# Kernel tuning notes

Measured on AMD Instinct MI355X. Metric: run time of the kernel, lower is better.

The kernel has to match this reference:

```python
import jax, jax.numpy as jnp
import numpy as np

# model dims
C_CH = 64      # channels C
M_DIM = 128    # state dim m
R = 8          # low-rank r
DG = 64        # token_dim d_g
CHUNK = 512    # chunk_len
B, H, W = 4, 256, 256


def setup_inputs() -> dict:
    key = jax.random.key(0)
    ks = jax.random.split(key, 12)
    n = jax.random.normal
    return {
        "x": n(ks[0], (B, C_CH, H, W), jnp.float32),
        "g": n(ks[1], (B, DG), jnp.float32),
        # 1x1 conv weights flattened to matrices
        "in_proj_w": n(ks[2], (M_DIM, C_CH), jnp.float32) * 0.05,
        "in_proj_b": jnp.zeros((M_DIM,), jnp.float32),
        "out_proj_w": n(ks[3], (C_CH, M_DIM), jnp.float32) * 0.05,  # Cbase; conv bias unused in forward
        "U_base": n(ks[4], (M_DIM, R), jnp.float32) * 0.02,
        "V_base": n(ks[5], (M_DIM, R), jnp.float32) * 0.02,
        "a_base": jnp.zeros((M_DIM,), jnp.float32),
        "mod_uv_w": n(ks[6], (2 * R, DG), jnp.float32) * 0.05,
        "mod_uv_b": jnp.zeros((2 * R,), jnp.float32),
        "mod_a_w": n(ks[7], (M_DIM, DG), jnp.float32) * 0.05,
        "mod_a_b": jnp.zeros((M_DIM,), jnp.float32),
        "mod_B_w": n(ks[8], (M_DIM, DG), jnp.float32) * 0.05,
        "mod_B_b": jnp.zeros((M_DIM,), jnp.float32),
        "mod_C_w": n(ks[9], (C_CH, DG), jnp.float32) * 0.05,
        "mod_C_b": jnp.zeros((C_CH,), jnp.float32),
        "h0": jnp.zeros((M_DIM,), jnp.float32),
    }


def reference(x, g, in_proj_w, in_proj_b, out_proj_w, U_base, V_base, a_base,
              mod_uv_w, mod_uv_b, mod_a_w, mod_a_b, mod_B_w, mod_B_b,
              mod_C_w, mod_C_b, h0):
    Bsz, Cch, Hh, Ww = x.shape
    # 1x1 conv in_proj
    x_proj = jnp.einsum('bchw,mc->bmhw', x, in_proj_w) + in_proj_b[None, :, None, None]
    # g-conditioned modulations
    uv = g @ mod_uv_w.T + mod_uv_b
    gU = jnp.clip(uv[:, :R], -0.5, 0.5)[:, None, :]          # (B,1,r)
    gV = jnp.clip(uv[:, R:], -0.5, 0.5)[:, None, :]          # (B,1,r)
    ga = jnp.clip(g @ mod_a_w.T + mod_a_b, -2.0, 2.0)        # (B,m)
    gB = jnp.clip(g @ mod_B_w.T + mod_B_b, -1.0, 1.0)        # (B,m)
    gC = jnp.clip(g @ mod_C_w.T + mod_C_b, -0.5, 0.5)        # (B,C)
    Ug = U_base[None] * (1.0 + gU)                            # (B,m,r)
    Vg = V_base[None] * (1.0 + gV)                            # (B,m,r)
    a = a_base[None] + ga                                     # (B,m)
    Cg = out_proj_w[None] * (1.0 + gC)[:, :, None]            # (B,C,m)

    L = Hh * Ww
    x_seq = x_proj.reshape(Bsz, M_DIM, L).transpose(0, 2, 1)  # (B,L,m)
    x_seq = x_seq * (1.0 + gB)[:, None, :]
    pad = (-L) % CHUNK
    if pad > 0:
        x_seq = jnp.pad(x_seq, ((0, 0), (0, pad), (0, 0)))
    Lp = L + pad
    Mch = Lp // CHUNK
    # (T, B, K, m): scan over time within chunks, chunks run in parallel
    x_chunks = x_seq.reshape(Bsz, Mch, CHUNK, M_DIM).transpose(2, 0, 1, 3)
    h_init = jnp.broadcast_to(h0, (Bsz, Mch, M_DIM))

    def step(h, xt):
        v = jnp.einsum('bmr,bkm->bkr', Vg, h)                 # V^T h
        Av = jnp.einsum('bmr,bkr->bkm', Ug, v)                # U (V^T h)
        h_new = jnp.clip(Av + h * a[:, None, :] + xt, -10.0, 10.0)
        yc = jnp.clip(jnp.einsum('bcm,bkm->bkc', Cg, h_new), -10.0, 10.0)
        return h_new, yc

    _, ys = jax.lax.scan(step, h_init, x_chunks)              # (T,B,K,C)
    out_flat = ys.transpose(1, 2, 0, 3).reshape(Bsz, Lp, Cch)[:, :L, :]
    return out_flat.transpose(0, 2, 1).reshape(Bsz, Cch, Hh, Ww)
```

## Files before the change

kernel.cpp:

```cpp
#include <hip/hip_runtime.h>
#include <hip/hip_fp16.h>

#define L_TOT 65536

#define WS_UG   0
#define WS_VG   4096
#define WS_A    8192
#define WS_GB1  8704
#define WS_WHP  12288
#define WS_WLP  16384
#define WS_CGP  32768
#define WS_XS   65536

typedef __attribute__((ext_vector_type(8))) short short8;
typedef __attribute__((ext_vector_type(4))) float f32x4;

__device__ __forceinline__ unsigned bf16rne(float f) {
    unsigned u = __builtin_bit_cast(unsigned, f);
    return (u + 0x7fffu + ((u >> 16) & 1u)) >> 16;
}
__device__ __forceinline__ float bfhi(unsigned u) {
    return __builtin_bit_cast(float, u << 16);
}

#define DPP_ROW(CT) \
    "v_add_f32_dpp %0, %0, %0 " CT "\n\t" \
    "v_add_f32_dpp %1, %1, %1 " CT "\n\t" \
    "v_add_f32_dpp %2, %2, %2 " CT "\n\t" \
    "v_add_f32_dpp %3, %3, %3 " CT "\n\t" \
    "v_add_f32_dpp %4, %4, %4 " CT "\n\t" \
    "v_add_f32_dpp %5, %5, %5 " CT "\n\t" \
    "v_add_f32_dpp %6, %6, %6 " CT "\n\t" \
    "v_add_f32_dpp %7, %7, %7 " CT "\n\t"

__global__ __launch_bounds__(128) void mod_kernel(
    const float* __restrict__ g, const float* __restrict__ in_proj_w,
    const float* __restrict__ U_base, const float* __restrict__ V_base,
    const float* __restrict__ a_base, const float* __restrict__ out_proj_w,
    const float* __restrict__ mod_uv_w, const float* __restrict__ mod_uv_b,
    const float* __restrict__ mod_a_w, const float* __restrict__ mod_a_b,
    const float* __restrict__ mod_B_w, const float* __restrict__ mod_B_b,
    const float* __restrict__ mod_C_w, const float* __restrict__ mod_C_b,
    float* __restrict__ ws)
{
    __shared__ float gsh[64];
    __shared__ float uvs[16];
    __shared__ float gCs[64];
    const int b = blockIdx.x, tid = threadIdx.x;
    if (tid < 64) gsh[tid] = g[b * 64 + tid];
    __syncthreads();
    if (tid < 16) {
        float s = mod_uv_b[tid];
        for (int d = 0; d < 64; ++d) s += mod_uv_w[tid * 64 + d] * gsh[d];
        uvs[tid] = fminf(0.5f, fmaxf(-0.5f, s));
    }
    float ga_v, gB_v;
    {
        float s = mod_a_b[tid];
        for (int d = 0; d < 64; ++d) s += mod_a_w[tid * 64 + d] * gsh[d];
        ga_v = fminf(2.0f, fmaxf(-2.0f, s));
    }
    {
        float s = mod_B_b[tid];
        for (int d = 0; d < 64; ++d) s += mod_B_w[tid * 64 + d] * gsh[d];
        gB_v = 1.0f + fminf(1.0f, fmaxf(-1.0f, s));
    }
    if (tid < 64) {
        float s = mod_C_b[tid];
        for (int d = 0; d < 64; ++d) s += mod_C_w[tid * 64 + d] * gsh[d];
        gCs[tid] = 1.0f + fminf(0.5f, fmaxf(-0.5f, s));
    }
    __syncthreads();
    for (int idx = tid; idx < 1024; idx += 128) {
        int m = idx >> 3, r = idx & 7;
        ws[WS_UG + (b * 128 + m) * 8 + r] = U_base[m * 8 + r] * (1.0f + uvs[r]);
        ws[WS_VG + (b * 128 + m) * 8 + r] = V_base[m * 8 + r] * (1.0f + uvs[8 + r]);
    }
    ws[WS_A   + b * 128 + tid] = a_base[tid] + ga_v;
    ws[WS_GB1 + b * 128 + tid] = gB_v;
    unsigned* CgP = (unsigned*)(ws + WS_CGP);
    for (int idx = tid; idx < 4096; idx += 128) {
        int c = idx >> 6, j = idx & 63;
        float s = gCs[c];
        float c0 = out_proj_w[c * 128 + 2 * j]     * s;
        float c1 = out_proj_w[c * 128 + 2 * j + 1] * s;
        CgP[(b * 64 + c) * 64 + j] = bf16rne(c0) | (bf16rne(c1) << 16);
    }
    if (b == 0) {
        unsigned* WhP = (unsigned*)(ws + WS_WHP);
        unsigned* WlP = (unsigned*)(ws + WS_WLP);
        for (int idx = tid; idx < 4096; idx += 128) {
            int m = idx >> 5, j = idx & 31;
            float w0 = in_proj_w[m * 64 + 2 * j];
            float w1 = in_proj_w[m * 64 + 2 * j + 1];
            unsigned u0 = bf16rne(w0), u1 = bf16rne(w1);
            WhP[idx] = u0 | (u1 << 16);
            float r0 = w0 - bfhi(u0);
            float r1 = w1 - bfhi(u1);
            WlP[idx] = bf16rne(r0) | (bf16rne(r1) << 16);
        }
    }
}

__global__ __launch_bounds__(256) void inproj_mfma(
    const float* __restrict__ x, const unsigned* __restrict__ WhP,
    const unsigned* __restrict__ WlP, const float* __restrict__ bias,
    const float* __restrict__ ws, unsigned* __restrict__ xs16)
{
    __shared__ __align__(16) unsigned XhS[64 * 36];
    __shared__ __align__(16) unsigned XlS[64 * 36];
    const int tid = threadIdx.x;
    const int b = blockIdx.y;
    const int l0 = blockIdx.x * 64;

    {
        const int l_st = tid & 63, cpg = tid >> 6;
        #pragma unroll
        for (int s = 0; s < 8; ++s) {
            int cp = cpg * 8 + s;
            float x0 = x[(size_t)(b * 64 + 2 * cp) * L_TOT + l0 + l_st];
            float x1 = x[(size_t)(b * 64 + 2 * cp + 1) * L_TOT + l0 + l_st];
            unsigned u0 = bf16rne(x0), u1 = bf16rne(x1);
            XhS[l_st * 36 + cp] = u0 | (u1 << 16);
            float r0 = x0 - bfhi(u0);
            float r1 = x1 - bfhi(u1);
            XlS[l_st * 36 + cp] = bf16rne(r0) | (bf16rne(r1) << 16);
        }
    }
    const int lane = tid & 63, wv = tid >> 6;
    const int row16 = lane & 15, grp = lane >> 4;

    short8 Ah[2][2], Al[2][2];
    #pragma unroll
    for (int t = 0; t < 2; ++t) {
        const int mrow = (2 * wv + t) * 16 + row16;
        #pragma unroll
        for (int kc = 0; kc < 2; ++kc) {
            Ah[t][kc] = __builtin_bit_cast(short8,
                *(const uint4*)(WhP + mrow * 32 + kc * 16 + grp * 4));
            Al[t][kc] = __builtin_bit_cast(short8,
                *(const uint4*)(WlP + mrow * 32 + kc * 16 + grp * 4));
        }
    }
    __syncthreads();

    #pragma unroll
    for (int ti = 0; ti < 4; ++ti) {
        const int lcol = ti * 16 + row16;
        short8 Bh[2], Bl[2];
        #pragma unroll
        for (int kc = 0; kc < 2; ++kc) {
            Bh[kc] = __builtin_bit_cast(short8,
                *(const uint4*)&XhS[lcol * 36 + kc * 16 + grp * 4]);
            Bl[kc] = __builtin_bit_cast(short8,
                *(const uint4*)&XlS[lcol * 36 + kc * 16 + grp * 4]);
        }
        #pragma unroll
        for (int t = 0; t < 2; ++t) {
            f32x4 acc = {0.f, 0.f, 0.f, 0.f};
            acc = __builtin_amdgcn_mfma_f32_16x16x32_bf16(Ah[t][0], Bh[0], acc, 0, 0, 0);
            acc = __builtin_amdgcn_mfma_f32_16x16x32_bf16(Ah[t][1], Bh[1], acc, 0, 0, 0);
            acc = __builtin_amdgcn_mfma_f32_16x16x32_bf16(Ah[t][0], Bl[0], acc, 0, 0, 0);
            acc = __builtin_amdgcn_mfma_f32_16x16x32_bf16(Ah[t][1], Bl[1], acc, 0, 0, 0);
            acc = __builtin_amdgcn_mfma_f32_16x16x32_bf16(Al[t][0], Bh[0], acc, 0, 0, 0);
            acc = __builtin_amdgcn_mfma_f32_16x16x32_bf16(Al[t][1], Bh[1], acc, 0, 0, 0);
            const int mb = (2 * wv + t) * 16 + 4 * grp;
            const int l = l0 + lcol;
            float4 bi = *(const float4*)(bias + mb);
            float4 gb = *(const float4*)(ws + WS_GB1 + b * 128 + mb);
            float v0 = (acc[0] + bi.x) * gb.x;
            float v1 = (acc[1] + bi.y) * gb.y;
            float v2 = (acc[2] + bi.z) * gb.z;
            float v3 = (acc[3] + bi.w) * gb.w;
            __half2 h01 = __floats2half2_rn(v0, v1);
            __half2 h23 = __floats2half2_rn(v2, v3);
            uint2 pk = {__builtin_bit_cast(unsigned, h01), __builtin_bit_cast(unsigned, h23)};
            *(uint2*)(xs16 + ((size_t)b * L_TOT + l) * 64 + (mb >> 1)) = pk;
        }
    }
}

__global__ __launch_bounds__(64, 1) void scan_kernel(
    const unsigned* __restrict__ xs16, const float* __restrict__ ws,
    const unsigned* __restrict__ CgP, const float* __restrict__ h0,
    float* __restrict__ out)
{
    __shared__ __align__(16) unsigned Hs[16 * 68];
    const int lane = threadIdx.x;
    const int bb = blockIdx.x >> 7, k = blockIdx.x & 127;
    const int m0 = 2 * lane;

    float Vg0[8], Vg1[8], Ug0[8], Ug1[8];
    {
        const float* vg = ws + WS_VG + (bb * 128 + m0) * 8;
        const float* ug = ws + WS_UG + (bb * 128 + m0) * 8;
        #pragma unroll
        for (int r = 0; r < 8; ++r) {
            Vg0[r] = vg[r]; Vg1[r] = vg[8 + r];
            Ug0[r] = ug[r]; Ug1[r] = ug[8 + r];
        }
    }
    const float a0 = ws[WS_A + bb * 128 + m0];
    const float a1 = ws[WS_A + bb * 128 + m0 + 1];
    float ha = h0[m0], hb = h0[m0 + 1];

    short8 Af[4][4];
    const int row16 = lane & 15, grp = lane >> 4;
    #pragma unroll
    for (int ct = 0; ct < 4; ++ct)
        #pragma unroll
        for (int kc = 0; kc < 4; ++kc) {
            const unsigned* p = CgP + (bb * 64 + ct * 16 + row16) * 64 + kc * 16 + grp * 4;
            Af[ct][kc] = __builtin_bit_cast(short8, *(const uint4*)p);
        }

    const unsigned* xsp = xs16 + ((size_t)bb * L_TOT + (size_t)k * 512) * 64 + lane;
    float* ob[4];
    #pragma unroll
    for (int ct = 0; ct < 4; ++ct)
        ob[ct] = out + (size_t)(bb * 64 + ct * 16 + grp * 4) * L_TOT + k * 512 + row16;

    unsigned xqA[16], xqB[16];

    auto prefetch = [&](unsigned (&xq)[16], int seg) {
        const unsigned* xb = xsp + (size_t)seg * 1024;
        #pragma unroll
        for (int i = 0; i < 16; ++i) xq[i] = xb[(size_t)i * 64];
    };
    auto do_seg = [&](const unsigned (&xq)[16], int t16) {
        #pragma unroll
        for (int i = 0; i < 16; ++i) {
            const float2 xv = __half22float2(__builtin_bit_cast(__half2, xq[i]));
            float p0 = fmaf(Vg1[0], hb, Vg0[0] * ha);
            float p1 = fmaf(Vg1[1], hb, Vg0[1] * ha);
            float p2 = fmaf(Vg1[2], hb, Vg0[2] * ha);
            float p3 = fmaf(Vg1[3], hb, Vg0[3] * ha);
            float p4 = fmaf(Vg1[4], hb, Vg0[4] * ha);
            float p5 = fmaf(Vg1[5], hb, Vg0[5] * ha);
            float p6 = fmaf(Vg1[6], hb, Vg0[6] * ha);
            float p7 = fmaf(Vg1[7], hb, Vg0[7] * ha);
            asm volatile(
                "s_nop 1\n\t"
                DPP_ROW("quad_perm:[1,0,3,2] row_mask:0xf bank_mask:0xf bound_ctrl:1")
                DPP_ROW("quad_perm:[2,3,0,1] row_mask:0xf bank_mask:0xf bound_ctrl:1")
                DPP_ROW("row_half_mirror row_mask:0xf bank_mask:0xf bound_ctrl:1")
                DPP_ROW("row_mirror row_mask:0xf bank_mask:0xf bound_ctrl:1")
                DPP_ROW("row_bcast:15 row_mask:0xa bank_mask:0xf")
                DPP_ROW("row_bcast:31 row_mask:0xc bank_mask:0xf")
                : "+v"(p0), "+v"(p1), "+v"(p2), "+v"(p3),
                  "+v"(p4), "+v"(p5), "+v"(p6), "+v"(p7));
            float v0 = __builtin_bit_cast(float, __builtin_amdgcn_readlane(__builtin_bit_cast(int, p0), 63));
            float v1 = __builtin_bit_cast(float, __builtin_amdgcn_readlane(__builtin_bit_cast(int, p1), 63));
            float v2 = __builtin_bit_cast(float, __builtin_amdgcn_readlane(__builtin_bit_cast(int, p2), 63));
            float v3 = __builtin_bit_cast(float, __builtin_amdgcn_readlane(__builtin_bit_cast(int, p3), 63));
            float v4 = __builtin_bit_cast(float, __builtin_amdgcn_readlane(__builtin_bit_cast(int, p4), 63));
            float v5 = __builtin_bit_cast(float, __builtin_amdgcn_readlane(__builtin_bit_cast(int, p5), 63));
            float v6 = __builtin_bit_cast(float, __builtin_amdgcn_readlane(__builtin_bit_cast(int, p6), 63));
            float v7 = __builtin_bit_cast(float, __builtin_amdgcn_readlane(__builtin_bit_cast(int, p7), 63));
            float q0 = fmaf(v1, Ug0[1], v0 * Ug0[0]);
            float q1 = fmaf(v3, Ug0[3], v2 * Ug0[2]);
            float q2 = fmaf(v5, Ug0[5], v4 * Ug0[4]);
            float q3 = fmaf(v7, Ug0[7], v6 * Ug0[6]);
            float av0 = (q0 + q1) + (q2 + q3);
            float s0 = fmaf(v1, Ug1[1], v0 * Ug1[0]);
            float s1 = fmaf(v3, Ug1[3], v2 * Ug1[2]);
            float s2 = fmaf(v5, Ug1[5], v4 * Ug1[4]);
            float s3 = fmaf(v7, Ug1[7], v6 * Ug1[6]);
            float av1 = (s0 + s1) + (s2 + s3);
            ha = fminf(10.0f, fmaxf(-10.0f, fmaf(a0, ha, av0) + xv.x));
            hb = fminf(10.0f, fmaxf(-10.0f, fmaf(a1, hb, av1) + xv.y));
            unsigned hp;
            asm("v_cvt_pk_bf16_f32 %0, %1, %2" : "=v"(hp) : "v"(ha), "v"(hb));
            Hs[i * 68 + lane] = hp;
        }
        short8 Bf[4];
        #pragma unroll
        for (int kc = 0; kc < 4; ++kc)
            Bf[kc] = __builtin_bit_cast(short8,
                *(const uint4*)&Hs[row16 * 68 + kc * 16 + grp * 4]);
        #pragma unroll
        for (int ct = 0; ct < 4; ++ct) {
            f32x4 acc = {0.0f, 0.0f, 0.0f, 0.0f};
            #pragma unroll
            for (int kc = 0; kc < 4; ++kc)
                acc = __builtin_amdgcn_mfma_f32_16x16x32_bf16(Af[ct][kc], Bf[kc], acc, 0, 0, 0);
            #pragma unroll
            for (int r = 0; r < 4; ++r) {
                float y = fminf(10.0f, fmaxf(-10.0f, acc[r]));
                ob[ct][(size_t)r * L_TOT + t16 * 16] = y;
            }
        }
    };

    prefetch(xqA, 0);
    #pragma unroll 1
    for (int t16 = 0; t16 < 32; t16 += 2) {
        prefetch(xqB, t16 + 1);
        do_seg(xqA, t16);
        prefetch(xqA, (t16 + 2) & 31);
        do_seg(xqB, t16 + 1);
    }
}

extern "C" void kernel_launch(void* const* d_in, const int* in_sizes, int n_in,
                              void* d_out, int out_size, void* d_ws, size_t ws_size,
                              hipStream_t stream) {
    const float* x          = (const float*)d_in[0];
    const float* g          = (const float*)d_in[1];
    const float* in_proj_w  = (const float*)d_in[2];
    const float* in_proj_b  = (const float*)d_in[3];
    const float* out_proj_w = (const float*)d_in[4];
    const float* U_base     = (const float*)d_in[5];
    const float* V_base     = (const float*)d_in[6];
    const float* a_base     = (const float*)d_in[7];
    const float* mod_uv_w   = (const float*)d_in[8];
    const float* mod_uv_b   = (const float*)d_in[9];
    const float* mod_a_w    = (const float*)d_in[10];
    const float* mod_a_b    = (const float*)d_in[11];
    const float* mod_B_w    = (const float*)d_in[12];
    const float* mod_B_b    = (const float*)d_in[13];
    const float* mod_C_w    = (const float*)d_in[14];
    const float* mod_C_b    = (const float*)d_in[15];
    const float* h0         = (const float*)d_in[16];
    float* out = (float*)d_out;
    float* ws  = (float*)d_ws;
    unsigned* xs16 = (unsigned*)(ws + WS_XS);

    hipLaunchKernelGGL(mod_kernel, dim3(4), dim3(128), 0, stream,
                       g, in_proj_w, U_base, V_base, a_base, out_proj_w,
                       mod_uv_w, mod_uv_b, mod_a_w, mod_a_b,
                       mod_B_w, mod_B_b, mod_C_w, mod_C_b, ws);
    hipLaunchKernelGGL(inproj_mfma, dim3(1024, 4), dim3(256), 0, stream,
                       x, (const unsigned*)(ws + WS_WHP), (const unsigned*)(ws + WS_WLP),
                       in_proj_b, ws, xs16);
    hipLaunchKernelGGL(scan_kernel, dim3(512), dim3(64), 0, stream,
                       xs16, ws, (const unsigned*)(ws + WS_CGP), h0, out);
}
```

Before: 172.1 us.

## Fuse in-projection into scan kernel with warp-specialized producer/scan/output pipeline

Result: slower. 193.5 us (+12.4%).

```diff
diff --git a/kernel.cpp b/kernel.cpp
--- a/kernel.cpp
+++ b/kernel.cpp
@@ -10,7 +10,6 @@
 #define WS_WHP  12288
 #define WS_WLP  16384
 #define WS_CGP  32768
-#define WS_XS   65536
 
 typedef __attribute__((ext_vector_type(8))) short short8;
 typedef __attribute__((ext_vector_type(4))) float f32x4;
@@ -102,96 +101,26 @@
     }
 }
 
-__global__ __launch_bounds__(256) void inproj_mfma(
+__global__ __launch_bounds__(192, 1) void fused_kernel(
     const float* __restrict__ x, const unsigned* __restrict__ WhP,
     const unsigned* __restrict__ WlP, const float* __restrict__ bias,
-    const float* __restrict__ ws, unsigned* __restrict__ xs16)
+    const float* __restrict__ ws, const unsigned* __restrict__ CgP,
+    const float* __restrict__ h0, float* __restrict__ out)
 {
-    __shared__ __align__(16) unsigned XhS[64 * 36];
-    __shared__ __align__(16) unsigned XlS[64 * 36];
+    __shared__ __align__(16) unsigned XhS[16 * 36];
+    __shared__ __align__(16) unsigned XlS[16 * 36];
+    __shared__ __align__(16) unsigned xp[2][64 * 17];
+    __shared__ __align__(16) unsigned Hs[2][16 * 68];
+
     const int tid = threadIdx.x;
-    const int b = blockIdx.y;
-    const int l0 = blockIdx.x * 64;
-
-    {
-        const int l_st = tid & 63, cpg = tid >> 6;
-        #pragma unroll
-        for (int s = 0; s < 8; ++s) {
-            int cp = cpg * 8 + s;
-            float x0 = x[(size_t)(b * 64 + 2 * cp) * L_TOT + l0 + l_st];
-            float x1 = x[(size_t)(b * 64 + 2 * cp + 1) * L_TOT + l0 + l_st];
-            unsigned u0 = bf16rne(x0), u1 = bf16rne(x1);
-            XhS[l_st * 36 + cp] = u0 | (u1 << 16);
-            float r0 = x0 - bfhi(u0);
-            float r1 = x1 - bfhi(u1);
-            XlS[l_st * 36 + cp] = bf16rne(r0) | (bf16rne(r1) << 16);
-        }
-    }
-    const int lane = tid & 63, wv = tid >> 6;
+    const int lane = tid & 63, wid = tid >> 6;
+    const int bb = blockIdx.x >> 7, kchunk = blockIdx.x & 127;
+    const size_t l0chunk = (size_t)kchunk * 512;
     const int row16 = lane & 15, grp = lane >> 4;
 
-    short8 Ah[2][2], Al[2][2];
-    #pragma unroll
-    for (int t = 0; t < 2; ++t) {
-        const int mrow = (2 * wv + t) * 16 + row16;
-        #pragma unroll
-        for (int kc = 0; kc < 2; ++kc) {
-            Ah[t][kc] = __builtin_bit_cast(short8,
-                *(const uint4*)(WhP + mrow * 32 + kc * 16 + grp * 4));
-            Al[t][kc] = __builtin_bit_cast(short8,
-                *(const uint4*)(WlP + mrow * 32 + kc * 16 + grp * 4));
-        }
-    }
-    __syncthreads();
-
-    #pragma unroll
-    for (int ti = 0; ti < 4; ++ti) {
-        const int lcol = ti * 16 + row16;
-        short8 Bh[2], Bl[2];
-        #pragma unroll
-        for (int kc = 0; kc < 2; ++kc) {
-            Bh[kc] = __builtin_bit_cast(short8,
-                *(const uint4*)&XhS[lcol * 36 + kc * 16 + grp * 4]);
-            Bl[kc] = __builtin_bit_cast(short8,
-                *(const uint4*)&XlS[lcol * 36 + kc * 16 + grp * 4]);
-        }
-        #pragma unroll
-        for (int t = 0; t < 2; ++t) {
-            f32x4 acc = {0.f, 0.f, 0.f, 0.f};
-            acc = __builtin_amdgcn_mfma_f32_16x16x32_bf16(Ah[t][0], Bh[0], acc, 0, 0, 0);
-            acc = __builtin_amdgcn_mfma_f32_16x16x32_bf16(Ah[t][1], Bh[1], acc, 0, 0, 0);
-            acc = __builtin_amdgcn_mfma_f32_16x16x32_bf16(Ah[t][0], Bl[0], acc, 0, 0, 0);
-            acc = __builtin_amdgcn_mfma_f32_16x16x32_bf16(Ah[t][1], Bl[1], acc, 0, 0, 0);
-            acc = __builtin_amdgcn_mfma_f32_16x16x32_bf16(Al[t][0], Bh[0], acc, 0, 0, 0);
-            acc = __builtin_amdgcn_mfma_f32_16x16x32_bf16(Al[t][1], Bh[1], acc, 0, 0, 0);
-            const int mb = (2 * wv + t) * 16 + 4 * grp;
-            const int l = l0 + lcol;
-            float4 bi = *(const float4*)(bias + mb);
-            float4 gb = *(const float4*)(ws + WS_GB1 + b * 128 + mb);
-            float v0 = (acc[0] + bi.x) * gb.x;
-            float v1 = (acc[1] + bi.y) * gb.y;
-            float v2 = (acc[2] + bi.z) * gb.z;
-            float v3 = (acc[3] + bi.w) * gb.w;
-            __half2 h01 = __floats2half2_rn(v0, v1);
-            __half2 h23 = __floats2half2_rn(v2, v3);
-            uint2 pk = {__builtin_bit_cast(unsigned, h01), __builtin_bit_cast(unsigned, h23)};
-            *(uint2*)(xs16 + ((size_t)b * L_TOT + l) * 64 + (mb >> 1)) = pk;
-        }
-    }
-}
-
-__global__ __launch_bounds__(64, 1) void scan_kernel(
-    const unsigned* __restrict__ xs16, const float* __restrict__ ws,
-    const unsigned* __restrict__ CgP, const float* __restrict__ h0,
-    float* __restrict__ out)
-{
-    __shared__ __align__(16) unsigned Hs[16 * 68];
-    const int lane = threadIdx.x;
-    const int bb = blockIdx.x >> 7, k = blockIdx.x & 127;
+    float Vg0[8], Vg1[8], Ug0[8], Ug1[8], a0 = 0.f, a1 = 0.f, ha = 0.f, hb = 0.f;
     const int m0 = 2 * lane;
-
-    float Vg0[8], Vg1[8], Ug0[8], Ug1[8];
-    {
+    if (wid == 0) {
         const float* vg = ws + WS_VG + (bb * 128 + m0) * 8;
         const float* ug = ws + WS_UG + (bb * 128 + m0) * 8;
         #pragma unroll
@@ -199,106 +128,151 @@
             Vg0[r] = vg[r]; Vg1[r] = vg[8 + r];
             Ug0[r] = ug[r]; Ug1[r] = ug[8 + r];
         }
-    }
-    const float a0 = ws[WS_A + bb * 128 + m0];
-    const float a1 = ws[WS_A + bb * 128 + m0 + 1];
-    float ha = h0[m0], hb = h0[m0 + 1];
-
+        a0 = ws[WS_A + bb * 128 + m0];
+        a1 = ws[WS_A + bb * 128 + m0 + 1];
+        ha = h0[m0]; hb = h0[m0 + 1];
+    }
     short8 Af[4][4];
-    const int row16 = lane & 15, grp = lane >> 4;
-    #pragma unroll
-    for (int ct = 0; ct < 4; ++ct)
-        #pragma unroll
-        for (int kc = 0; kc < 4; ++kc) {
-            const unsigned* p = CgP + (bb * 64 + ct * 16 + row16) * 64 + kc * 16 + grp * 4;
-            Af[ct][kc] = __builtin_bit_cast(short8, *(const uint4*)p);
-        }
-
-    const unsigned* xsp = xs16 + ((size_t)bb * L_TOT + (size_t)k * 512) * 64 + lane;
     float* ob[4];
-    #pragma unroll
-    for (int ct = 0; ct < 4; ++ct)
-        ob[ct] = out + (size_t)(bb * 64 + ct * 16 + grp * 4) * L_TOT + k * 512 + row16;
-
-    unsigned xqA[16], xqB[16];
-
-    auto prefetch = [&](unsigned (&xq)[16], int seg) {
-        const unsigned* xb = xsp + (size_t)seg * 1024;
-        #pragma unroll
-        for (int i = 0; i < 16; ++i) xq[i] = xb[(size_t)i * 64];
-    };
-    auto do_seg = [&](const unsigned (&xq)[16], int t16) {
-        #pragma unroll
-        for (int i = 0; i < 16; ++i) {
-            const float2 xv = __half22float2(__builtin_bit_cast(__half2, xq[i]));
-            float p0 = fmaf(Vg1[0], hb, Vg0[0] * ha);
-            float p1 = fmaf(Vg1[1], hb, Vg0[1] * ha);
-            float p2 = fmaf(Vg1[2], hb, Vg0[2] * ha);
-            float p3 = fmaf(Vg1[3], hb, Vg0[3] * ha);
-            float p4 = fmaf(Vg1[4], hb, Vg0[4] * ha);
-            float p5 = fmaf(Vg1[5], hb, Vg0[5] * ha);
-            float p6 = fmaf(Vg1[6], hb, Vg0[6] * ha);
-            float p7 = fmaf(Vg1[7], hb, Vg0[7] * ha);
-            asm volatile(
-                "s_nop 1\n\t"
-                DPP_ROW("quad_perm:[1,0,3,2] row_mask:0xf bank_mask:0xf bound_ctrl:1")
-                DPP_ROW("quad_perm:[2,3,0,1] row_mask:0xf bank_mask:0xf bound_ctrl:1")
-                DPP_ROW("row_half_mirror row_mask:0xf bank_mask:0xf bound_ctrl:1")
-                DPP_ROW("row_mirror row_mask:0xf bank_mask:0xf bound_ctrl:1")
-                DPP_ROW("row_bcast:15 row_mask:0xa bank_mask:0xf")
-                DPP_ROW("row_bcast:31 row_mask:0xc bank_mask:0xf")
-                : "+v"(p0), "+v"(p1), "+v"(p2), "+v"(p3),
-                  "+v"(p4), "+v"(p5), "+v"(p6), "+v"(p7));
-            float v0 = __builtin_bit_cast(float, __builtin_amdgcn_readlane(__builtin_bit_cast(int, p0), 63));
-            float v1 = __builtin_bit_cast(float, __builtin_amdgcn_readlane(__builtin_bit_cast(int, p1), 63));
-            float v2 = __builtin_bit_cast(float, __builtin_amdgcn_readlane(__builtin_bit_cast(int, p2), 63));
-            float v3 = __builtin_bit_cast(float, __builtin_amdgcn_readlane(__builtin_bit_cast(int, p3), 63));
-            float v4 = __builtin_bit_cast(float, __builtin_amdgcn_readlane(__builtin_bit_cast(int, p4), 63));
-            float v5 = __builtin_bit_cast(float, __builtin_amdgcn_readlane(__builtin_bit_cast(int, p5), 63));
-            float v6 = __builtin_bit_cast(float, __builtin_amdgcn_readlane(__builtin_bit_cast(int, p6), 63));
-            float v7 = __builtin_bit_cast(float, __builtin_amdgcn_readlane(__builtin_bit_cast(int, p7), 63));
-            float q0 = fmaf(v1, Ug0[1], v0 * Ug0[0]);
-            float q1 = fmaf(v3, Ug0[3], v2 * Ug0[2]);
-            float q2 = fmaf(v5, Ug0[5], v4 * Ug0[4]);
-            float q3 = fmaf(v7, Ug0[7], v6 * Ug0[6]);
-            float av0 = (q0 + q1) + (q2 + q3);
-            float s0 = fmaf(v1, Ug1[1], v0 * Ug1[0]);
-            float s1 = fmaf(v3, Ug1[3], v2 * Ug1[2]);
-            float s2 = fmaf(v5, Ug1[5], v4 * Ug1[4]);
-            float s3 = fmaf(v7, Ug1[7], v6 * Ug1[6]);
-            float av1 = (s0 + s1) + (s2 + s3);
-            ha = fminf(10.0f, fmaxf(-10.0f, fmaf(a0, ha, av0) + xv.x));
-            hb = fminf(10.0f, fmaxf(-10.0f, fmaf(a1, hb, av1) + xv.y));
-            unsigned hp;
-            asm("v_cvt_pk_bf16_f32 %0, %1, %2" : "=v"(hp) : "v"(ha), "v"(hb));
-            Hs[i * 68 + lane] = hp;
-        }
-        short8 Bf[4];
-        #pragma unroll
-        for (int kc = 0; kc < 4; ++kc)
-            Bf[kc] = __builtin_bit_cast(short8,
-                *(const uint4*)&Hs[row16 * 68 + kc * 16 + grp * 4]);
+    if (wid == 2) {
         #pragma unroll
         for (int ct = 0; ct < 4; ++ct) {
-            f32x4 acc = {0.0f, 0.0f, 0.0f, 0.0f};
+            #pragma unroll
+            for (int kc = 0; kc < 4; ++kc) {
+                const unsigned* p = CgP + (bb * 64 + ct * 16 + row16) * 64 + kc * 16 + grp * 4;
+                Af[ct][kc] = __builtin_bit_cast(short8, *(const uint4*)p);
+            }
+            ob[ct] = out + (size_t)(bb * 64 + ct * 16 + grp * 4) * L_TOT + l0chunk + row16;
+        }
+    }
+
+    for (int k = -1; k <= 32; ++k) {
+        if (wid == 1 && k <= 30) {
+            const int s = k + 1;
+            const float* xb = x + (size_t)(bb * 64) * L_TOT + l0chunk + s * 16 + row16;
+            #pragma unroll
+            for (int t = 0; t < 8; ++t) {
+                int cp = grp * 8 + t;
+                float x0 = xb[(size_t)(2 * cp) * L_TOT];
+                float x1 = xb[(size_t)(2 * cp + 1) * L_TOT];
+                unsigned u0 = bf16rne(x0), u1 = bf16rne(x1);
+                XhS[row16 * 36 + cp] = u0 | (u1 << 16);
+                float r0 = x0 - bfhi(u0);
+                float r1 = x1 - bfhi(u1);
+                XlS[row16 * 36 + cp] = bf16rne(r0) | (bf16rne(r1) << 16);
+            }
+            asm volatile("s_waitcnt lgkmcnt(0)" ::: "memory");
+            short8 Bh[2], Bl[2];
+            #pragma unroll
+            for (int kc = 0; kc < 2; ++kc) {
+                Bh[kc] = __builtin_bit_cast(short8,
+                    *(const uint4*)&XhS[row16 * 36 + kc * 16 + grp * 4]);
+                Bl[kc] = __builtin_bit_cast(short8,
+                    *(const uint4*)&XlS[row16 * 36 + kc * 16 + grp * 4]);
+            }
+            unsigned* xpd = xp[s & 1];
+            #pragma unroll
+            for (int mt = 0; mt < 8; ++mt) {
+                const int mrow = mt * 16 + row16;
+                short8 Ah0 = __builtin_bit_cast(short8, *(const uint4*)(WhP + mrow * 32 + grp * 4));
+                short8 Ah1 = __builtin_bit_cast(short8, *(const uint4*)(WhP + mrow * 32 + 16 + grp * 4));
+                short8 Al0 = __builtin_bit_cast(short8, *(const uint4*)(WlP + mrow * 32 + grp * 4));
+                short8 Al1 = __builtin_bit_cast(short8, *(const uint4*)(WlP + mrow * 32 + 16 + grp * 4));
+                f32x4 acc = {0.f, 0.f, 0.f, 0.f};
+                acc = __builtin_amdgcn_mfma_f32_16x16x32_bf16(Ah0, Bh[0], acc, 0, 0, 0);
+                acc = __builtin_amdgcn_mfma_f32_16x16x32_bf16(Ah1, Bh[1], acc, 0, 0, 0);
+                acc = __builtin_amdgcn_mfma_f32_16x16x32_bf16(Ah0, Bl[0], acc, 0, 0, 0);
+                acc = __builtin_amdgcn_mfma_f32_16x16x32_bf16(Ah1, Bl[1], acc, 0, 0, 0);
+                acc = __builtin_amdgcn_mfma_f32_16x16x32_bf16(Al0, Bh[0], acc, 0, 0, 0);
+                acc = __builtin_amdgcn_mfma_f32_16x16x32_bf16(Al1, Bh[1], acc, 0, 0, 0);
+                const int mb = mt * 16 + 4 * grp;
+                float4 bi = *(const float4*)(bias + mb);
+                float4 gb = *(const float4*)(ws + WS_GB1 + bb * 128 + mb);
+                float v0 = (acc[0] + bi.x) * gb.x;
+                float v1 = (acc[1] + bi.y) * gb.y;
+                float v2 = (acc[2] + bi.z) * gb.z;
+                float v3 = (acc[3] + bi.w) * gb.w;
+                __half2 h01 = __floats2half2_rn(v0, v1);
+                __half2 h23 = __floats2half2_rn(v2, v3);
+                const int mp = mb >> 1;
+                xpd[mp * 17 + row16]       = __builtin_bit_cast(unsigned, h01);
+                xpd[(mp + 1) * 17 + row16] = __builtin_bit_cast(unsigned, h23);
+            }
+        }
+        if (wid == 0 && k >= 0 && k <= 31) {
+            const unsigned* xpk = xp[k & 1];
+            unsigned* Hk = Hs[k & 1];
+            unsigned xq[16];
+            #pragma unroll
+            for (int i = 0; i < 16; ++i) xq[i] = xpk[lane * 17 + i];
+            #pragma unroll
+            for (int i = 0; i < 16; ++i) {
+                const float2 xv = __half22float2(__builtin_bit_cast(__half2, xq[i]));
+                float p0 = fmaf(Vg1[0], hb, Vg0[0] * ha);
+                float p1 = fmaf(Vg1[1], hb, Vg0[1] * ha);
+                float p2 = fmaf(Vg1[2], hb, Vg0[2] * ha);
+                float p3 = fmaf(Vg1[3], hb, Vg0[3] * ha);
+                float p4 = fmaf(Vg1[4], hb, Vg0[4] * ha);
+                float p5 = fmaf(Vg1[5], hb, Vg0[5] * ha);
+                float p6 = fmaf(Vg1[6], hb, Vg0[6] * ha);
+                float p7 = fmaf(Vg1[7], hb, Vg0[7] * ha);
+                asm volatile(
+                    "s_nop 1\n\t"
+                    DPP_ROW("quad_perm:[1,0,3,2] row_mask:0xf bank_mask:0xf bound_ctrl:1")
+                    DPP_ROW("quad_perm:[2,3,0,1] row_mask:0xf bank_mask:0xf bound_ctrl:1")
+                    DPP_ROW("row_half_mirror row_mask:0xf bank_mask:0xf bound_ctrl:1")
+                    DPP_ROW("row_mirror row_mask:0xf bank_mask:0xf bound_ctrl:1")
+                    DPP_ROW("row_bcast:15 row_mask:0xa bank_mask:0xf")
+                    DPP_ROW("row_bcast:31 row_mask:0xc bank_mask:0xf")
+                    : "+v"(p0), "+v"(p1), "+v"(p2), "+v"(p3),
+                      "+v"(p4), "+v"(p5), "+v"(p6), "+v"(p7));
+                float v0 = __builtin_bit_cast(float, __builtin_amdgcn_readlane(__builtin_bit_cast(int, p0), 63));
+                float v1 = __builtin_bit_cast(float, __builtin_amdgcn_readlane(__builtin_bit_cast(int, p1), 63));
+                float v2 = __builtin_bit_cast(float, __builtin_amdgcn_readlane(__builtin_bit_cast(int, p2), 63));
+                float v3 = __builtin_bit_cast(float, __builtin_amdgcn_readlane(__builtin_bit_cast(int, p3), 63));
+                float v4 = __builtin_bit_cast(float, __builtin_amdgcn_readlane(__builtin_bit_cast(int, p4), 63));
+                float v5 = __builtin_bit_cast(float, __builtin_amdgcn_readlane(__builtin_bit_cast(int, p5), 63));
+                float v6 = __builtin_bit_cast(float, __builtin_amdgcn_readlane(__builtin_bit_cast(int, p6), 63));
+                float v7 = __builtin_bit_cast(float, __builtin_amdgcn_readlane(__builtin_bit_cast(int, p7), 63));
+                float q0 = fmaf(v1, Ug0[1], v0 * Ug0[0]);
+                float q1 = fmaf(v3, Ug0[3], v2 * Ug0[2]);
+                float q2 = fmaf(v5, Ug0[5], v4 * Ug0[4]);
+                float q3 = fmaf(v7, Ug0[7], v6 * Ug0[6]);
+                float av0 = (q0 + q1) + (q2 + q3);
+                float s0 = fmaf(v1, Ug1[1], v0 * Ug1[0]);
+                float s1 = fmaf(v3, Ug1[3], v2 * Ug1[2]);
+                float s2 = fmaf(v5, Ug1[5], v4 * Ug1[4]);
+                float s3 = fmaf(v7, Ug1[7], v6 * Ug1[6]);
+                float av1 = (s0 + s1) + (s2 + s3);
+                ha = fminf(10.0f, fmaxf(-10.0f, fmaf(a0, ha, av0) + xv.x));
+                hb = fminf(10.0f, fmaxf(-10.0f, fmaf(a1, hb, av1) + xv.y));
+                unsigned hp;
+                asm("v_cvt_pk_bf16_f32 %0, %1, %2" : "=v"(hp) : "v"(ha), "v"(hb));
+                Hk[i * 68 + lane] = hp;
+            }
+        }
+        if (wid == 2 && k >= 1) {
+            const int s = k - 1;
+            const unsigned* Hp = Hs[s & 1];
+            short8 Bf[4];
             #pragma unroll
             for (int kc = 0; kc < 4; ++kc)
-                acc = __builtin_amdgcn_mfma_f32_16x16x32_bf16(Af[ct][kc], Bf[kc], acc, 0, 0, 0);
-            #pragma unroll
-            for (int r = 0; r < 4; ++r) {
-                float y = fminf(10.0f, fmaxf(-10.0f, acc[r]));
-                ob[ct][(size_t)r * L_TOT + t16 * 16] = y;
-            }
-        }
-    };
-
-    prefetch(xqA, 0);
-    #pragma unroll 1
-    for (int t16 = 0; t16 < 32; t16 += 2) {
-        prefetch(xqB, t16 + 1);
-        do_seg(xqA, t16);
-        prefetch(xqA, (t16 + 2) & 31);
-        do_seg(xqB, t16 + 1);
+                Bf[kc] = __builtin_bit_cast(short8,
+                    *(const uint4*)&Hp[row16 * 68 + kc * 16 + grp * 4]);
+            #pragma unroll
+            for (int ct = 0; ct < 4; ++ct) {
+                f32x4 acc = {0.0f, 0.0f, 0.0f, 0.0f};
+                #pragma unroll
+                for (int kc = 0; kc < 4; ++kc)
+                    acc = __builtin_amdgcn_mfma_f32_16x16x32_bf16(Af[ct][kc], Bf[kc], acc, 0, 0, 0);
+                #pragma unroll
+                for (int r = 0; r < 4; ++r) {
+                    float y = fminf(10.0f, fmaxf(-10.0f, acc[r]));
+                    ob[ct][(size_t)r * L_TOT + s * 16] = y;
+                }
+            }
+        }
+        __syncthreads();
     }
 }
 
@@ -324,15 +298,12 @@
     const float* h0         = (const float*)d_in[16];
     float* out = (float*)d_out;
     float* ws  = (float*)d_ws;
-    unsigned* xs16 = (unsigned*)(ws + WS_XS);
 
     hipLaunchKernelGGL(mod_kernel, dim3(4), dim3(128), 0, stream,
                        g, in_proj_w, U_base, V_base, a_base, out_proj_w,
                        mod_uv_w, mod_uv_b, mod_a_w, mod_a_b,
                        mod_B_w, mod_B_b, mod_C_w, mod_C_b, ws);
-    hipLaunchKernelGGL(inproj_mfma, dim3(1024, 4), dim3(256), 0, stream,
+    hipLaunchKernelGGL(fused_kernel, dim3(512), dim3(192), 0, stream,
                        x, (const unsigned*)(ws + WS_WHP), (const unsigned*)(ws + WS_WLP),
-                       in_proj_b, ws, xs16);
-    hipLaunchKernelGGL(scan_kernel, dim3(512), dim3(64), 0, stream,
-                       xs16, ws, (const unsigned*)(ws + WS_CGP), h0, out);
-}
+                       in_proj_b, ws, (const unsigned*)(ws + WS_CGP), h0, out);
+}
```

## Compute per-step V^T h with split-fp16 MFMA instead of DPP reductions

Applied to the files above, without the earlier changes.

Result: slower. 188.3 us (+9.4%).

```diff
diff --git a/kernel.cpp b/kernel.cpp
--- a/kernel.cpp
+++ b/kernel.cpp
@@ -14,6 +14,7 @@
 
 typedef __attribute__((ext_vector_type(8))) short short8;
 typedef __attribute__((ext_vector_type(4))) float f32x4;
+typedef _Float16 half8 __attribute__((ext_vector_type(8)));
 
 __device__ __forceinline__ unsigned bf16rne(float f) {
     unsigned u = __builtin_bit_cast(unsigned, f);
@@ -22,16 +23,10 @@
 __device__ __forceinline__ float bfhi(unsigned u) {
     return __builtin_bit_cast(float, u << 16);
 }
-
-#define DPP_ROW(CT) \
-    "v_add_f32_dpp %0, %0, %0 " CT "\n\t" \
-    "v_add_f32_dpp %1, %1, %1 " CT "\n\t" \
-    "v_add_f32_dpp %2, %2, %2 " CT "\n\t" \
-    "v_add_f32_dpp %3, %3, %3 " CT "\n\t" \
-    "v_add_f32_dpp %4, %4, %4 " CT "\n\t" \
-    "v_add_f32_dpp %5, %5, %5 " CT "\n\t" \
-    "v_add_f32_dpp %6, %6, %6 " CT "\n\t" \
-    "v_add_f32_dpp %7, %7, %7 " CT "\n\t"
+__device__ __forceinline__ unsigned f16pk(float a, float b) {
+    __half2 h = __floats2half2_rn(a, b);
+    return __builtin_bit_cast(unsigned, h);
+}
 
 __global__ __launch_bounds__(128) void mod_kernel(
     const float* __restrict__ g, const float* __restrict__ in_proj_w,
@@ -84,7 +79,7 @@
         float s = gCs[c];
         float c0 = out_proj_w[c * 128 + 2 * j]     * s;
         float c1 = out_proj_w[c * 128 + 2 * j + 1] * s;
-        CgP[(b * 64 + c) * 64 + j] = bf16rne(c0) | (bf16rne(c1) << 16);
+        CgP[(b * 64 + c) * 64 + j] = f16pk(c0, c1);
     }
     if (b == 0) {
         unsigned* WhP = (unsigned*)(ws + WS_WHP);
@@ -172,9 +167,7 @@
             float v1 = (acc[1] + bi.y) * gb.y;
             float v2 = (acc[2] + bi.z) * gb.z;
             float v3 = (acc[3] + bi.w) * gb.w;
-            __half2 h01 = __floats2half2_rn(v0, v1);
-            __half2 h23 = __floats2half2_rn(v2, v3);
-            uint2 pk = {__builtin_bit_cast(unsigned, h01), __builtin_bit_cast(unsigned, h23)};
+            uint2 pk = {f16pk(v0, v1), f16pk(v2, v3)};
             *(uint2*)(xs16 + ((size_t)b * L_TOT + l) * 64 + (mb >> 1)) = pk;
         }
     }
@@ -189,29 +182,55 @@
     const int lane = threadIdx.x;
     const int bb = blockIdx.x >> 7, k = blockIdx.x & 127;
     const int m0 = 2 * lane;
-
-    float Vg0[8], Vg1[8], Ug0[8], Ug1[8];
+    const int row16 = lane & 15, grp = lane >> 4;
+
+    float UgA0[4], UgB0[4], UgA1[4], UgB1[4];
     {
-        const float* vg = ws + WS_VG + (bb * 128 + m0) * 8;
         const float* ug = ws + WS_UG + (bb * 128 + m0) * 8;
-        #pragma unroll
-        for (int r = 0; r < 8; ++r) {
-            Vg0[r] = vg[r]; Vg1[r] = vg[8 + r];
-            Ug0[r] = ug[r]; Ug1[r] = ug[8 + r];
+        float Ug0[8], Ug1[8];
+        #pragma unroll
+        for (int r = 0; r < 8; ++r) { Ug0[r] = ug[r]; Ug1[r] = ug[8 + r]; }
+        const bool oddg = (grp & 1) != 0;
+        #pragma unroll
+        for (int q = 0; q < 4; ++q) {
+            UgA0[q] = oddg ? Ug0[4 + q] : Ug0[q];
+            UgB0[q] = oddg ? Ug0[q]     : Ug0[4 + q];
+            UgA1[q] = oddg ? Ug1[4 + q] : Ug1[q];
+            UgB1[q] = oddg ? Ug1[q]     : Ug1[4 + q];
         }
     }
     const float a0 = ws[WS_A + bb * 128 + m0];
     const float a1 = ws[WS_A + bb * 128 + m0 + 1];
     float ha = h0[m0], hb = h0[m0 + 1];
 
-    short8 Af[4][4];
-    const int row16 = lane & 15, grp = lane >> 4;
+    half8 AVh[4], AVl[4];
+    #pragma unroll
+    for (int kc = 0; kc < 4; ++kc) {
+        unsigned uh[4], ul[4];
+        #pragma unroll
+        for (int q = 0; q < 4; ++q) {
+            int k0 = kc * 32 + grp * 8 + 2 * q;
+            float f0 = ws[WS_VG + (bb * 128 + k0) * 8 + (row16 & 7)];
+            float f1 = ws[WS_VG + (bb * 128 + k0 + 1) * 8 + (row16 & 7)];
+            __half g0 = __float2half(f0), g1 = __float2half(f1);
+            uh[q] = (unsigned)__half_as_ushort(g0) | ((unsigned)__half_as_ushort(g1) << 16);
+            __half r0 = __float2half(f0 - __half2float(g0));
+            __half r1 = __float2half(f1 - __half2float(g1));
+            ul[q] = (unsigned)__half_as_ushort(r0) | ((unsigned)__half_as_ushort(r1) << 16);
+        }
+        uint4 th = {uh[0], uh[1], uh[2], uh[3]};
+        uint4 tl = {ul[0], ul[1], ul[2], ul[3]};
+        AVh[kc] = __builtin_bit_cast(half8, th);
+        AVl[kc] = __builtin_bit_cast(half8, tl);
+    }
+
+    half8 Af[4][4];
     #pragma unroll
     for (int ct = 0; ct < 4; ++ct)
         #pragma unroll
         for (int kc = 0; kc < 4; ++kc) {
             const unsigned* p = CgP + (bb * 64 + ct * 16 + row16) * 64 + kc * 16 + grp * 4;
-            Af[ct][kc] = __builtin_bit_cast(short8, *(const uint4*)p);
+            Af[ct][kc] = __builtin_bit_cast(half8, *(const uint4*)p);
         }
 
     const unsigned* xsp = xs16 + ((size_t)bb * L_TOT + (size_t)k * 512) * 64 + lane;
@@ -221,69 +240,74 @@
         ob[ct] = out + (size_t)(bb * 64 + ct * 16 + grp * 4) * L_TOT + k * 512 + row16;
 
     unsigned xqA[16], xqB[16];
-
     auto prefetch = [&](unsigned (&xq)[16], int seg) {
         const unsigned* xb = xsp + (size_t)seg * 1024;
         #pragma unroll
         for (int i = 0; i < 16; ++i) xq[i] = xb[(size_t)i * 64];
     };
+
+    Hs[15 * 68 + lane] = f16pk(ha, hb);
+    uint4 Bv[4];
+    #pragma unroll
+    for (int kc = 0; kc < 4; ++kc)
+        Bv[kc] = *(const uint4*)&Hs[15 * 68 + kc * 16 + grp * 4];
+
     auto do_seg = [&](const unsigned (&xq)[16], int t16) {
         #pragma unroll
         for (int i = 0; i < 16; ++i) {
             const float2 xv = __half22float2(__builtin_bit_cast(__half2, xq[i]));
-            float p0 = fmaf(Vg1[0], hb, Vg0[0] * ha);
-            float p1 = fmaf(Vg1[1], hb, Vg0[1] * ha);
-            float p2 = fmaf(Vg1[2], hb, Vg0[2] * ha);
-            float p3 = fmaf(Vg1[3], hb, Vg0[3] * ha);
-            float p4 = fmaf(Vg1[4], hb, Vg0[4] * ha);
-            float p5 = fmaf(Vg1[5], hb, Vg0[5] * ha);
-            float p6 = fmaf(Vg1[6], hb, Vg0[6] * ha);
-            float p7 = fmaf(Vg1[7], hb, Vg0[7] * ha);
-            asm volatile(
-                "s_nop 1\n\t"
-                DPP_ROW("quad_perm:[1,0,3,2] row_mask:0xf bank_mask:0xf bound_ctrl:1")
-                DPP_ROW("quad_perm:[2,3,0,1] row_mask:0xf bank_mask:0xf bound_ctrl:1")
-                DPP_ROW("row_half_mirror row_mask:0xf bank_mask:0xf bound_ctrl:1")
-                DPP_ROW("row_mirror row_mask:0xf bank_mask:0xf bound_ctrl:1")
-                DPP_ROW("row_bcast:15 row_mask:0xa bank_mask:0xf")
-                DPP_ROW("row_bcast:31 row_mask:0xc bank_mask:0xf")
-                : "+v"(p0), "+v"(p1), "+v"(p2), "+v"(p3),
-                  "+v"(p4), "+v"(p5), "+v"(p6), "+v"(p7));
-            float v0 = __builtin_bit_cast(float, __builtin_amdgcn_readlane(__builtin_bit_cast(int, p0), 63));
-            float v1 = __builtin_bit_cast(float, __builtin_amdgcn_readlane(__builtin_bit_cast(int, p1), 63));
-            float v2 = __builtin_bit_cast(float, __builtin_amdgcn_readlane(__builtin_bit_cast(int, p2), 63));
-            float v3 = __builtin_bit_cast(float, __builtin_amdgcn_readlane(__builtin_bit_cast(int, p3), 63));
-            float v4 = __builtin_bit_cast(float, __builtin_amdgcn_readlane(__builtin_bit_cast(int, p4), 63));
-            float v5 = __builtin_bit_cast(float, __builtin_amdgcn_readlane(__builtin_bit_cast(int, p5), 63));
-            float v6 = __builtin_bit_cast(float, __builtin_amdgcn_readlane(__builtin_bit_cast(int, p6), 63));
-            float v7 = __builtin_bit_cast(float, __builtin_amdgcn_readlane(__builtin_bit_cast(int, p7), 63));
-            float q0 = fmaf(v1, Ug0[1], v0 * Ug0[0]);
-            float q1 = fmaf(v3, Ug0[3], v2 * Ug0[2]);
-            float q2 = fmaf(v5, Ug0[5], v4 * Ug0[4]);
-            float q3 = fmaf(v7, Ug0[7], v6 * Ug0[6]);
-            float av0 = (q0 + q1) + (q2 + q3);
-            float s0 = fmaf(v1, Ug1[1], v0 * Ug1[0]);
-            float s1 = fmaf(v3, Ug1[3], v2 * Ug1[2]);
-            float s2 = fmaf(v5, Ug1[5], v4 * Ug1[4]);
-            float s3 = fmaf(v7, Ug1[7], v6 * Ug1[6]);
-            float av1 = (s0 + s1) + (s2 + s3);
+            f32x4 aH = {0.f, 0.f, 0.f, 0.f};
+            f32x4 aL = {0.f, 0.f, 0.f, 0.f};
+            #pragma unroll
+            for (int kc = 0; kc < 4; ++kc) {
+                half8 B = __builtin_bit_cast(half8, Bv[kc]);
+                aH = __builtin_amdgcn_mfma_f32_16x16x32_f16(AVh[kc], B, aH, 0, 0, 0);
+                aL = __builtin_amdgcn_mfma_f32_16x16x32_f16(AVl[kc], B, aL, 0, 0, 0);
+            }
+            float vo0 = aH[0] + aL[0];
+            float vo1 = aH[1] + aL[1];
+            float vo2 = aH[2] + aL[2];
+            float vo3 = aH[3] + aL[3];
+            int o0 = __builtin_amdgcn_ds_swizzle(__builtin_bit_cast(int, vo0), 0x401F);
+            int o1 = __builtin_amdgcn_ds_swizzle(__builtin_bit_cast(int, vo1), 0x401F);
+            int o2 = __builtin_amdgcn_ds_swizzle(__builtin_bit_cast(int, vo2), 0x401F);
+            int o3 = __builtin_amdgcn_ds_swizzle(__builtin_bit_cast(int, vo3), 0x401F);
+            float av0 = fmaf(vo1, UgA0[1], vo0 * UgA0[0]);
+            av0 = fmaf(vo2, UgA0[2], av0);
+            av0 = fmaf(vo3, UgA0[3], av0);
+            float av1 = fmaf(vo1, UgA1[1], vo0 * UgA1[0]);
+            av1 = fmaf(vo2, UgA1[2], av1);
+            av1 = fmaf(vo3, UgA1[3], av1);
+            float ot0 = __builtin_bit_cast(float, o0);
+            float ot1 = __builtin_bit_cast(float, o1);
+            float ot2 = __builtin_bit_cast(float, o2);
+            float ot3 = __builtin_bit_cast(float, o3);
+            av0 = fmaf(ot0, UgB0[0], av0);
+            av0 = fmaf(ot1, UgB0[1], av0);
+            av0 = fmaf(ot2, UgB0[2], av0);
+            av0 = fmaf(ot3, UgB0[3], av0);
+            av1 = fmaf(ot0, UgB1[0], av1);
+            av1 = fmaf(ot1, UgB1[1], av1);
+            av1 = fmaf(ot2, UgB1[2], av1);
+            av1 = fmaf(ot3, UgB1[3], av1);
             ha = fminf(10.0f, fmaxf(-10.0f, fmaf(a0, ha, av0) + xv.x));
             hb = fminf(10.0f, fmaxf(-10.0f, fmaf(a1, hb, av1) + xv.y));
-            unsigned hp;
-            asm("v_cvt_pk_bf16_f32 %0, %1, %2" : "=v"(hp) : "v"(ha), "v"(hb));
-            Hs[i * 68 + lane] = hp;
-        }
-        short8 Bf[4];
+            Hs[i * 68 + lane] = f16pk(ha, hb);
+            #pragma unroll
+            for (int kc = 0; kc < 4; ++kc)
+                Bv[kc] = *(const uint4*)&Hs[i * 68 + kc * 16 + grp * 4];
+        }
+        half8 Bf[4];
         #pragma unroll
         for (int kc = 0; kc < 4; ++kc)
-            Bf[kc] = __builtin_bit_cast(short8,
+            Bf[kc] = __builtin_bit_cast(half8,
                 *(const uint4*)&Hs[row16 * 68 + kc * 16 + grp * 4]);
         #pragma unroll
         for (int ct = 0; ct < 4; ++ct) {
             f32x4 acc = {0.0f, 0.0f, 0.0f, 0.0f};
             #pragma unroll
             for (int kc = 0; kc < 4; ++kc)
-                acc = __builtin_amdgcn_mfma_f32_16x16x32_bf16(Af[ct][kc], Bf[kc], acc, 0, 0, 0);
+                acc = __builtin_amdgcn_mfma_f32_16x16x32_f16(Af[ct][kc], Bf[kc], acc, 0, 0, 0);
             #pragma unroll
             for (int r = 0; r < 4; ++r) {
                 float y = fminf(10.0f, fmaxf(-10.0f, acc[r]));
```
